# Kernel tuning notes

Hardware: AMD Instinct MI355X
Metric: run time of the kernel (lower is better)

The kernel has to match this reference:

```python
import jax, jax.numpy as jnp
import numpy as np

B, T, D = 8, 4096, 64

def setup_inputs() -> dict:
    key = jax.random.key(0)
    k1, k2 = jax.random.split(key)
    inputs = jax.random.normal(k1, (B, T, D), dtype=jnp.float32)
    # keras 'random_normal' initializer: stddev 0.05
    W = jax.random.normal(k2, (D, D), dtype=jnp.float32) * 0.05
    return {"inputs": inputs, "W": W}

def reference(inputs, W):
    # q = inputs @ W               : [B,T,D]
    # a = q @ inputs^T             : [B,T,T] (no scaling, bias b unused in original)
    # out = softmax(a, -1) @ inputs: [B,T,D]
    q = jnp.einsum('btd,de->bte', inputs, W)
    scores = jnp.einsum('btd,bsd->bts', q, inputs)
    attn = jax.nn.softmax(scores, axis=-1)
    return jnp.einsum('bts,bsd->btd', attn, inputs)
```

## Files before the change

kernel.cpp:

```cpp
#include <hip/hip_runtime.h>

typedef _Float16 f16;
typedef _Float16 f16x8 __attribute__((ext_vector_type(8)));
typedef __bf16 bf16x8 __attribute__((ext_vector_type(8)));
typedef float floatx4 __attribute__((ext_vector_type(4)));
typedef unsigned short u16;

#define B_N   8
#define T_SEQ 4096
#define DIM   64
#define QT    64
#define NIT   32
#define XSTR  72
#define LOG2E 1.44269504f
#define FRAG  512

#if __has_builtin(__builtin_amdgcn_exp2f)
#define EXP2(x) __builtin_amdgcn_exp2f(x)
#else
#define EXP2(x) exp2f(x)
#endif

typedef __attribute__((address_space(1))) const void gvoid;
typedef __attribute__((address_space(3))) void svoid;

__launch_bounds__(256, 4)
__global__ void prep_kernel(const float* __restrict__ X, const float* __restrict__ W,
                            u16* __restrict__ Kswz, u16* __restrict__ Qswz,
                            u16* __restrict__ Vswz) {
  __shared__ __attribute__((aligned(16))) u16 Xs[32 * XSTR];
  __shared__ __attribute__((aligned(16))) u16 Wt[DIM * XSTR];
  __shared__ __attribute__((aligned(16))) u16 Qs[2][16 * XSTR];
  const int tid = threadIdx.x;
  const int lane = tid & 63, w = tid >> 6, qd = lane >> 4, ln = lane & 15;
  const int b = blockIdx.y;
  const int tau = blockIdx.x;
  const long xbase = ((long)b * T_SEQ + tau * 32) * DIM;

  {
    const int r = tid >> 3, c0 = (tid & 7) * 8;
    float v[8];
    *(float4*)&v[0] = *(const float4*)(X + xbase + (long)r * DIM + c0);
    *(float4*)&v[4] = *(const float4*)(X + xbase + (long)r * DIM + c0 + 4);
    u16 h[8];
#pragma unroll
    for (int j = 0; j < 8; j++) h[j] = __builtin_bit_cast(u16, (f16)v[j]);
    *(uint4*)&Xs[r * XSTR + c0] = *(uint4*)&h[0];
    const int r2 = tid >> 2, c2 = (tid & 3) * 16;
    float wv[16];
#pragma unroll
    for (int i = 0; i < 4; i++)
      *(float4*)&wv[i * 4] = *(const float4*)(W + r2 * DIM + c2 + i * 4);
#pragma unroll
    for (int j = 0; j < 16; j++) Wt[(c2 + j) * XSTR + r2] = __builtin_bit_cast(u16, (f16)wv[j]);
  }
  __syncthreads();

  if (w == 0) {
#pragma unroll
    for (int ct = 0; ct < 2; ct++) {
      const int krow = (ln >> 2) * 8 + ct * 4 + (ln & 3);
      const long F = ((long)b * 128 + tau) * 2 + ct;
#pragma unroll
      for (int ks = 0; ks < 2; ks++) {
        f16x8 kv = *(const f16x8*)&Xs[krow * XSTR + ks * 32 + qd * 8];
        *(f16x8*)(Kswz + (F * 2 + ks) * FRAG + lane * 8) = kv;
      }
    }
    {
      const long Cb = (long)b * 4 + 0;
      bf16x8 vv;
#pragma unroll
      for (int j = 0; j < 8; j++) {
        f16 hv = __builtin_bit_cast(f16, Xs[(qd * 8 + j) * XSTR + 0 * 16 + ln]);
        vv[j] = (__bf16)(float)hv;
      }
      *(bf16x8*)(Vswz + (Cb * (T_SEQ / 32) + tau) * FRAG + lane * 8) = vv;
    }
  } else if (w == 1) {
#pragma unroll
    for (int db = 1; db < 4; db++) {
      const long Cb = (long)b * 4 + db;
      bf16x8 vv;
#pragma unroll
      for (int j = 0; j < 8; j++) {
        f16 hv = __builtin_bit_cast(f16, Xs[(qd * 8 + j) * XSTR + db * 16 + ln]);
        vv[j] = (__bf16)(float)hv;
      }
      *(bf16x8*)(Vswz + (Cb * (T_SEQ / 32) + tau) * FRAG + lane * 8) = vv;
    }
  } else {
    const int h2 = w - 2;
    const int rq = h2 * 16;
    floatx4 acc[4];
#pragma unroll
    for (int ct = 0; ct < 4; ct++) acc[ct] = (floatx4)0.0f;
#pragma unroll
    for (int ks = 0; ks < 2; ks++) {
      f16x8 aX = *(const f16x8*)&Xs[(rq + ln) * XSTR + ks * 32 + qd * 8];
#pragma unroll
      for (int ct = 0; ct < 4; ct++) {
        f16x8 bW = *(const f16x8*)&Wt[(ct * 16 + ln) * XSTR + ks * 32 + qd * 8];
        acc[ct] = __builtin_amdgcn_mfma_f32_16x16x32_f16(aX, bW, acc[ct], 0, 0, 0);
      }
    }
#pragma unroll
    for (int ct = 0; ct < 4; ct++)
#pragma unroll
      for (int r = 0; r < 4; r++)
        Qs[h2][(qd * 4 + r) * XSTR + ct * 16 + ln] =
            __builtin_bit_cast(u16, (f16)(acc[ct][r] * LOG2E));
    const long R = (long)b * (T_SEQ / 16) + tau * 2 + h2;
#pragma unroll
    for (int ks = 0; ks < 2; ks++) {
      f16x8 qv = *(const f16x8*)&Qs[h2][ln * XSTR + ks * 32 + qd * 8];
      *(f16x8*)(Qswz + (R * 2 + ks) * FRAG + lane * 8) = qv;
    }
  }
}

__launch_bounds__(512, 4)
__global__ void attn_kernel(const u16* __restrict__ Kswz, const u16* __restrict__ Qswz,
                            const u16* __restrict__ Vswz, float* __restrict__ out) {
  __shared__ __attribute__((aligned(16))) char smem[35840];
  __shared__ float lpart[8][32];
  float* Opart = (float*)smem;

  const int tid = threadIdx.x;
  const int lane = tid & 63;
  const int w = tid >> 6;
  const int qd = lane >> 4;
  const int ln = lane & 15;
  const int wg = w >> 2;
  const int wk = w & 3;
  const int bid = blockIdx.x;
  const int b = bid & 7;
  const int q0 = (bid >> 3) * QT;
  const long bbase = (long)b * T_SEQ * DIM;

  f16x8 aQ[2][2];
#pragma unroll
  for (int rb = 0; rb < 2; rb++)
#pragma unroll
    for (int ks = 0; ks < 2; ks++)
      aQ[rb][ks] = *(const f16x8*)(Qswz +
          (((long)b * (T_SEQ / 16) + (q0 >> 4) + wg * 2 + rb) * 2 + ks) * FRAG + lane * 8);

  const char* gKw = (const char*)Kswz + (long)b * 524288 + (long)w * 2048 + lane * 16;
  const char* gV = (const char*)Vswz + (long)b * 524288 + (long)wk * 1024 + lane * 16;

#define STAGE(bufv, t)                                                                  \
  do {                                                                                  \
    const char* g = gKw + (long)(t) * 16384;                                            \
    char* l = smem + (bufv) * 16384 + w * 2048;                                         \
    __builtin_amdgcn_global_load_lds((gvoid*)(g), (svoid*)(l), 16, 0, 0);               \
    __builtin_amdgcn_global_load_lds((gvoid*)(g + 1024), (svoid*)(l + 1024), 16, 0, 0); \
  } while (0)

  floatx4 O[2][4];
  float lacc[2] = {0.f, 0.f};
#pragma unroll
  for (int rb = 0; rb < 2; rb++)
#pragma unroll
    for (int db = 0; db < 4; db++) O[rb][db] = (floatx4)0.0f;

  STAGE(0, 0);
  __syncthreads();

  int buf = 0;
#pragma unroll 1
  for (int t = 0; t < NIT; t++) {
    bf16x8 bV[4];
#pragma unroll
    for (int db = 0; db < 4; db++)
      bV[db] = *(const bf16x8*)(gV + (long)t * 4096 + (long)db * 131072);

    if (t + 1 < NIT) STAGE(buf ^ 1, t + 1);

    const char* Kb = smem + buf * 16384 + wk * 4096;
    f16x8 bK[2][2];
#pragma unroll
    for (int ct = 0; ct < 2; ct++)
#pragma unroll
      for (int ks = 0; ks < 2; ks++)
        bK[ct][ks] = *(const f16x8*)(Kb + (ct * 2 + ks) * 1024 + lane * 16);

    floatx4 St[2][2];
#pragma unroll
    for (int ct = 0; ct < 2; ct++)
#pragma unroll
      for (int rb = 0; rb < 2; rb++) St[ct][rb] = (floatx4)0.0f;
    __builtin_amdgcn_s_setprio(1);
#pragma unroll
    for (int ks = 0; ks < 2; ks++)
#pragma unroll
      for (int ct = 0; ct < 2; ct++)
#pragma unroll
        for (int rb = 0; rb < 2; rb++)
          St[ct][rb] = __builtin_amdgcn_mfma_f32_16x16x32_f16(bK[ct][ks], aQ[rb][ks], St[ct][rb], 0, 0, 0);
    __builtin_amdgcn_s_setprio(0);

    bf16x8 pk[2];
#pragma unroll
    for (int rb = 0; rb < 2; rb++) {
      float ps = 0.f;
#pragma unroll
      for (int ct = 0; ct < 2; ct++)
#pragma unroll
        for (int r = 0; r < 4; r++) {
          float p = EXP2(St[ct][rb][r]);
          ps += p;
          pk[rb][ct * 4 + r] = (__bf16)p;
        }
      lacc[rb] += ps;
    }

    __builtin_amdgcn_s_setprio(1);
#pragma unroll
    for (int rb = 0; rb < 2; rb++)
#pragma unroll
      for (int db = 0; db < 4; db++)
        O[rb][db] = __builtin_amdgcn_mfma_f32_16x16x32_bf16(pk[rb], bV[db], O[rb][db], 0, 0, 0);
    __builtin_amdgcn_s_setprio(0);

    __syncthreads();
    buf ^= 1;
  }

#pragma unroll
  for (int rb = 0; rb < 2; rb++) {
    float v = lacc[rb];
    v += __shfl_xor(v, 16, 64);
    v += __shfl_xor(v, 32, 64);
    if (qd == 0) lpart[w][rb * 16 + ln] = v;
  }

#pragma unroll
  for (int rb = 0; rb < 2; rb++) {
    __syncthreads();
#pragma unroll
    for (int db = 0; db < 4; db++)
#pragma unroll
      for (int r = 0; r < 4; r++)
        Opart[(w * 16 + qd * 4 + r) * 68 + db * 16 + ln] = O[rb][db][r];
    __syncthreads();
    const int wg2 = tid >> 8;
    const int q2 = (tid >> 4) & 15;
    const int d0 = (tid & 15) * 4;
    float4 s = *(const float4*)&Opart[((wg2 * 4 + 0) * 16 + q2) * 68 + d0];
    const float4 s1 = *(const float4*)&Opart[((wg2 * 4 + 1) * 16 + q2) * 68 + d0];
    const float4 s2 = *(const float4*)&Opart[((wg2 * 4 + 2) * 16 + q2) * 68 + d0];
    const float4 s3 = *(const float4*)&Opart[((wg2 * 4 + 3) * 16 + q2) * 68 + d0];
    float l = lpart[wg2 * 4 + 0][rb * 16 + q2] + lpart[wg2 * 4 + 1][rb * 16 + q2] +
              lpart[wg2 * 4 + 2][rb * 16 + q2] + lpart[wg2 * 4 + 3][rb * 16 + q2];
    const float inv = 1.0f / l;
    float4 o;
    o.x = (s.x + s1.x + s2.x + s3.x) * inv;
    o.y = (s.y + s1.y + s2.y + s3.y) * inv;
    o.z = (s.z + s1.z + s2.z + s3.z) * inv;
    o.w = (s.w + s1.w + s2.w + s3.w) * inv;
    *(float4*)(out + bbase + (long)(q0 + wg2 * 32 + rb * 16 + q2) * DIM + d0) = o;
  }
#undef STAGE
}

extern "C" void kernel_launch(void* const* d_in, const int* in_sizes, int n_in,
                              void* d_out, int out_size, void* d_ws, size_t ws_size,
                              hipStream_t stream) {
  const float* X = (const float*)d_in[0];
  const float* W = (const float*)d_in[1];
  float* out = (float*)d_out;
  const size_t SZ = (size_t)B_N * T_SEQ * DIM * 2;
  u16* Kswz = (u16*)d_ws;
  u16* Qswz = (u16*)((char*)d_ws + SZ);
  u16* Vswz = (u16*)((char*)d_ws + 2 * SZ);
  prep_kernel<<<dim3(T_SEQ / 32, B_N), 256, 0, stream>>>(X, W, Kswz, Qswz, Vswz);
  attn_kernel<<<dim3(B_N * (T_SEQ / QT)), 512, 0, stream>>>(Kswz, Qswz, Vswz, out);
}
```

Measured before the change: 104.6 us.

## Halve attention query tile to 32 rows, one 16-row block per wave

Reduces the per-block query tile from 64 to 32 rows, so each wave handles a single 16-row query block instead of two. The grid doubles to 1024 blocks, which gives more parallelism across CUs and lowers register pressure. In exchange each K/V tile staged into LDS and loaded from global memory is reused by half as many queries, so total K/V traffic doubles, and per-iteration MFMA work per sync shrinks, raising the relative cost of barriers.

```diff
diff --git a/kernel.cpp b/kernel.cpp
--- a/kernel.cpp
+++ b/kernel.cpp
@@ -9,7 +9,7 @@
 #define B_N   8
 #define T_SEQ 4096
 #define DIM   64
-#define QT    64
+#define QT    32
 #define NIT   32
 #define XSTR  72
 #define LOG2E 1.44269504f
@@ -123,7 +123,7 @@
 __global__ void attn_kernel(const u16* __restrict__ Kswz, const u16* __restrict__ Qswz,
                             const u16* __restrict__ Vswz, float* __restrict__ out) {
   __shared__ __attribute__((aligned(16))) char smem[35840];
-  __shared__ float lpart[8][32];
+  __shared__ float lpart[8][16];
   float* Opart = (float*)smem;
 
   const int tid = threadIdx.x;
@@ -131,20 +131,18 @@
   const int w = tid >> 6;
   const int qd = lane >> 4;
   const int ln = lane & 15;
-  const int wg = w >> 2;
+  const int qh = w >> 2;
   const int wk = w & 3;
   const int bid = blockIdx.x;
   const int b = bid & 7;
   const int q0 = (bid >> 3) * QT;
   const long bbase = (long)b * T_SEQ * DIM;
 
-  f16x8 aQ[2][2];
-#pragma unroll
-  for (int rb = 0; rb < 2; rb++)
-#pragma unroll
-    for (int ks = 0; ks < 2; ks++)
-      aQ[rb][ks] = *(const f16x8*)(Qswz +
-          (((long)b * (T_SEQ / 16) + (q0 >> 4) + wg * 2 + rb) * 2 + ks) * FRAG + lane * 8);
+  f16x8 aQ[2];
+#pragma unroll
+  for (int ks = 0; ks < 2; ks++)
+    aQ[ks] = *(const f16x8*)(Qswz +
+        (((long)b * (T_SEQ / 16) + (q0 >> 4) + qh) * 2 + ks) * FRAG + lane * 8);
 
   const char* gKw = (const char*)Kswz + (long)b * 524288 + (long)w * 2048 + lane * 16;
   const char* gV = (const char*)Vswz + (long)b * 524288 + (long)wk * 1024 + lane * 16;
@@ -157,12 +155,10 @@
     __builtin_amdgcn_global_load_lds((gvoid*)(g + 1024), (svoid*)(l + 1024), 16, 0, 0); \
   } while (0)
 
-  floatx4 O[2][4];
-  float lacc[2] = {0.f, 0.f};
-#pragma unroll
-  for (int rb = 0; rb < 2; rb++)
-#pragma unroll
-    for (int db = 0; db < 4; db++) O[rb][db] = (floatx4)0.0f;
+  floatx4 O[4];
+  float lacc = 0.f;
+#pragma unroll
+  for (int db = 0; db < 4; db++) O[db] = (floatx4)0.0f;
 
   STAGE(0, 0);
   __syncthreads();
@@ -185,81 +181,73 @@
       for (int ks = 0; ks < 2; ks++)
         bK[ct][ks] = *(const f16x8*)(Kb + (ct * 2 + ks) * 1024 + lane * 16);
 
-    floatx4 St[2][2];
-#pragma unroll
-    for (int ct = 0; ct < 2; ct++)
-#pragma unroll
-      for (int rb = 0; rb < 2; rb++) St[ct][rb] = (floatx4)0.0f;
+    floatx4 St[2];
+    St[0] = (floatx4)0.0f;
+    St[1] = (floatx4)0.0f;
     __builtin_amdgcn_s_setprio(1);
 #pragma unroll
     for (int ks = 0; ks < 2; ks++)
 #pragma unroll
       for (int ct = 0; ct < 2; ct++)
-#pragma unroll
-        for (int rb = 0; rb < 2; rb++)
-          St[ct][rb] = __builtin_amdgcn_mfma_f32_16x16x32_f16(bK[ct][ks], aQ[rb][ks], St[ct][rb], 0, 0, 0);
+        St[ct] = __builtin_amdgcn_mfma_f32_16x16x32_f16(bK[ct][ks], aQ[ks], St[ct], 0, 0, 0);
     __builtin_amdgcn_s_setprio(0);
 
-    bf16x8 pk[2];
-#pragma unroll
-    for (int rb = 0; rb < 2; rb++) {
+    bf16x8 pk;
+    {
       float ps = 0.f;
 #pragma unroll
       for (int ct = 0; ct < 2; ct++)
 #pragma unroll
         for (int r = 0; r < 4; r++) {
-          float p = EXP2(St[ct][rb][r]);
+          float p = EXP2(St[ct][r]);
           ps += p;
-          pk[rb][ct * 4 + r] = (__bf16)p;
+          pk[ct * 4 + r] = (__bf16)p;
         }
-      lacc[rb] += ps;
+      lacc += ps;
     }
 
     __builtin_amdgcn_s_setprio(1);
 #pragma unroll
-    for (int rb = 0; rb < 2; rb++)
-#pragma unroll
-      for (int db = 0; db < 4; db++)
-        O[rb][db] = __builtin_amdgcn_mfma_f32_16x16x32_bf16(pk[rb], bV[db], O[rb][db], 0, 0, 0);
+    for (int db = 0; db < 4; db++)
+      O[db] = __builtin_amdgcn_mfma_f32_16x16x32_bf16(pk, bV[db], O[db], 0, 0, 0);
     __builtin_amdgcn_s_setprio(0);
 
     __syncthreads();
     buf ^= 1;
   }
 
-#pragma unroll
-  for (int rb = 0; rb < 2; rb++) {
-    float v = lacc[rb];
+  {
+    float v = lacc;
     v += __shfl_xor(v, 16, 64);
     v += __shfl_xor(v, 32, 64);
-    if (qd == 0) lpart[w][rb * 16 + ln] = v;
-  }
-
-#pragma unroll
-  for (int rb = 0; rb < 2; rb++) {
-    __syncthreads();
-#pragma unroll
-    for (int db = 0; db < 4; db++)
-#pragma unroll
-      for (int r = 0; r < 4; r++)
-        Opart[(w * 16 + qd * 4 + r) * 68 + db * 16 + ln] = O[rb][db][r];
-    __syncthreads();
-    const int wg2 = tid >> 8;
-    const int q2 = (tid >> 4) & 15;
+    if (qd == 0) lpart[w][ln] = v;
+  }
+
+  __syncthreads();
+#pragma unroll
+  for (int db = 0; db < 4; db++)
+#pragma unroll
+    for (int r = 0; r < 4; r++)
+      Opart[(w * 16 + qd * 4 + r) * 68 + db * 16 + ln] = O[db][r];
+  __syncthreads();
+  {
+    const int ql = tid >> 4;
     const int d0 = (tid & 15) * 4;
-    float4 s = *(const float4*)&Opart[((wg2 * 4 + 0) * 16 + q2) * 68 + d0];
-    const float4 s1 = *(const float4*)&Opart[((wg2 * 4 + 1) * 16 + q2) * 68 + d0];
-    const float4 s2 = *(const float4*)&Opart[((wg2 * 4 + 2) * 16 + q2) * 68 + d0];
-    const float4 s3 = *(const float4*)&Opart[((wg2 * 4 + 3) * 16 + q2) * 68 + d0];
-    float l = lpart[wg2 * 4 + 0][rb * 16 + q2] + lpart[wg2 * 4 + 1][rb * 16 + q2] +
-              lpart[wg2 * 4 + 2][rb * 16 + q2] + lpart[wg2 * 4 + 3][rb * 16 + q2];
+    const int qh2 = ql >> 4;
+    const int q2 = ql & 15;
+    float4 s = *(const float4*)&Opart[((qh2 * 4 + 0) * 16 + q2) * 68 + d0];
+    const float4 s1 = *(const float4*)&Opart[((qh2 * 4 + 1) * 16 + q2) * 68 + d0];
+    const float4 s2 = *(const float4*)&Opart[((qh2 * 4 + 2) * 16 + q2) * 68 + d0];
+    const float4 s3 = *(const float4*)&Opart[((qh2 * 4 + 3) * 16 + q2) * 68 + d0];
+    float l = lpart[qh2 * 4 + 0][q2] + lpart[qh2 * 4 + 1][q2] +
+              lpart[qh2 * 4 + 2][q2] + lpart[qh2 * 4 + 3][q2];
     const float inv = 1.0f / l;
     float4 o;
     o.x = (s.x + s1.x + s2.x + s3.x) * inv;
     o.y = (s.y + s1.y + s2.y + s3.y) * inv;
     o.z = (s.z + s1.z + s2.z + s3.z) * inv;
     o.w = (s.w + s1.w + s2.w + s3.w) * inv;
-    *(float4*)(out + bbase + (long)(q0 + wg2 * 32 + rb * 16 + q2) * DIM + d0) = o;
+    *(float4*)(out + bbase + (long)(q0 + ql) * DIM + d0) = o;
   }
 #undef STAGE
 }
```

New measurement: 119.6 us. 1.14x slower.

## Split attention key range in two blocks and combine with a reduce kernel

Applied to the files above, without the earlier changes.

Splits each query tile's key/value sweep into two halves processed by separate blocks, doubling the grid from 512 to 1024 blocks. Each block writes unnormalized partial outputs and row sums to workspace, and a new reduce kernel adds the two halves and normalizes. This aims to improve occupancy across the many compute units, since 512 blocks may underfill the GPU. In exchange it adds an extra kernel launch and extra global traffic for the partials. The split relies on the scores being safe to exponentiate without a running max.

```diff
diff --git a/kernel.cpp b/kernel.cpp
--- a/kernel.cpp
+++ b/kernel.cpp
@@ -10,7 +10,6 @@
 #define T_SEQ 4096
 #define DIM   64
 #define QT    64
-#define NIT   32
 #define XSTR  72
 #define LOG2E 1.44269504f
 #define FRAG  512
@@ -119,9 +118,11 @@
   }
 }
 
+template <int SPLIT>
 __launch_bounds__(512, 4)
 __global__ void attn_kernel(const u16* __restrict__ Kswz, const u16* __restrict__ Qswz,
-                            const u16* __restrict__ Vswz, float* __restrict__ out) {
+                            const u16* __restrict__ Vswz, float* __restrict__ out,
+                            float* __restrict__ Op, float* __restrict__ Lp) {
   __shared__ __attribute__((aligned(16))) char smem[35840];
   __shared__ float lpart[8][32];
   float* Opart = (float*)smem;
@@ -135,7 +136,10 @@
   const int wk = w & 3;
   const int bid = blockIdx.x;
   const int b = bid & 7;
-  const int q0 = (bid >> 3) * QT;
+  const int h = SPLIT ? ((bid >> 3) & 1) : 0;
+  const int g = SPLIT ? (bid >> 4) : (bid >> 3);
+  const int q0 = g * QT;
+  const int NITL = SPLIT ? 16 : 32;
   const long bbase = (long)b * T_SEQ * DIM;
 
   f16x8 aQ[2][2];
@@ -146,15 +150,17 @@
       aQ[rb][ks] = *(const f16x8*)(Qswz +
           (((long)b * (T_SEQ / 16) + (q0 >> 4) + wg * 2 + rb) * 2 + ks) * FRAG + lane * 8);
 
-  const char* gKw = (const char*)Kswz + (long)b * 524288 + (long)w * 2048 + lane * 16;
-  const char* gV = (const char*)Vswz + (long)b * 524288 + (long)wk * 1024 + lane * 16;
+  const char* gKw = (const char*)Kswz + (long)b * 524288 + (long)h * 262144 +
+                    (long)w * 2048 + lane * 16;
+  const char* gV = (const char*)Vswz + (long)b * 524288 + (long)h * 65536 +
+                   (long)wk * 1024 + lane * 16;
 
 #define STAGE(bufv, t)                                                                  \
   do {                                                                                  \
-    const char* g = gKw + (long)(t) * 16384;                                            \
-    char* l = smem + (bufv) * 16384 + w * 2048;                                         \
-    __builtin_amdgcn_global_load_lds((gvoid*)(g), (svoid*)(l), 16, 0, 0);               \
-    __builtin_amdgcn_global_load_lds((gvoid*)(g + 1024), (svoid*)(l + 1024), 16, 0, 0); \
+    const char* g_ = gKw + (long)(t) * 16384;                                           \
+    char* l_ = smem + (bufv) * 16384 + w * 2048;                                        \
+    __builtin_amdgcn_global_load_lds((gvoid*)(g_), (svoid*)(l_), 16, 0, 0);             \
+    __builtin_amdgcn_global_load_lds((gvoid*)(g_ + 1024), (svoid*)(l_ + 1024), 16, 0, 0); \
   } while (0)
 
   floatx4 O[2][4];
@@ -169,13 +175,13 @@
 
   int buf = 0;
 #pragma unroll 1
-  for (int t = 0; t < NIT; t++) {
+  for (int t = 0; t < NITL; t++) {
     bf16x8 bV[4];
 #pragma unroll
     for (int db = 0; db < 4; db++)
       bV[db] = *(const bf16x8*)(gV + (long)t * 4096 + (long)db * 131072);
 
-    if (t + 1 < NIT) STAGE(buf ^ 1, t + 1);
+    if (t + 1 < NITL) STAGE(buf ^ 1, t + 1);
 
     const char* Kb = smem + buf * 16384 + wk * 4096;
     f16x8 bK[2][2];
@@ -247,21 +253,55 @@
     const int wg2 = tid >> 8;
     const int q2 = (tid >> 4) & 15;
     const int d0 = (tid & 15) * 4;
+    const int ql = wg2 * 32 + rb * 16 + q2;
     float4 s = *(const float4*)&Opart[((wg2 * 4 + 0) * 16 + q2) * 68 + d0];
     const float4 s1 = *(const float4*)&Opart[((wg2 * 4 + 1) * 16 + q2) * 68 + d0];
     const float4 s2 = *(const float4*)&Opart[((wg2 * 4 + 2) * 16 + q2) * 68 + d0];
     const float4 s3 = *(const float4*)&Opart[((wg2 * 4 + 3) * 16 + q2) * 68 + d0];
     float l = lpart[wg2 * 4 + 0][rb * 16 + q2] + lpart[wg2 * 4 + 1][rb * 16 + q2] +
               lpart[wg2 * 4 + 2][rb * 16 + q2] + lpart[wg2 * 4 + 3][rb * 16 + q2];
-    const float inv = 1.0f / l;
     float4 o;
-    o.x = (s.x + s1.x + s2.x + s3.x) * inv;
-    o.y = (s.y + s1.y + s2.y + s3.y) * inv;
-    o.z = (s.z + s1.z + s2.z + s3.z) * inv;
-    o.w = (s.w + s1.w + s2.w + s3.w) * inv;
-    *(float4*)(out + bbase + (long)(q0 + wg2 * 32 + rb * 16 + q2) * DIM + d0) = o;
+    o.x = s.x + s1.x + s2.x + s3.x;
+    o.y = s.y + s1.y + s2.y + s3.y;
+    o.z = s.z + s1.z + s2.z + s3.z;
+    o.w = s.w + s1.w + s2.w + s3.w;
+    if (SPLIT) {
+      *(float4*)(Op + (long)bid * (QT * DIM) + ql * DIM + d0) = o;
+      if (d0 == 0) Lp[(long)bid * QT + ql] = l;
+    } else {
+      const float inv = 1.0f / l;
+      o.x *= inv; o.y *= inv; o.z *= inv; o.w *= inv;
+      *(float4*)(out + bbase + (long)(q0 + ql) * DIM + d0) = o;
+    }
   }
 #undef STAGE
+}
+
+__launch_bounds__(256, 8)
+__global__ void reduce_kernel(const float* __restrict__ Op, const float* __restrict__ Lp,
+                              float* __restrict__ out) {
+  const int rb = blockIdx.x;
+  const int b = rb & 7, g = rb >> 3;
+  const int bid0 = g * 16 + b;
+  const int bid1 = g * 16 + 8 + b;
+  const long p0 = (long)bid0 * (QT * DIM);
+  const long p1 = (long)bid1 * (QT * DIM);
+  const long obase = ((long)b * T_SEQ + (long)g * QT) * DIM;
+#pragma unroll
+  for (int i = 0; i < 4; i++) {
+    const int lin4 = i * 256 + threadIdx.x;
+    const int q = lin4 >> 4;
+    const int d0 = (lin4 & 15) * 4;
+    float4 a = *(const float4*)(Op + p0 + (long)lin4 * 4);
+    float4 c = *(const float4*)(Op + p1 + (long)lin4 * 4);
+    const float inv = 1.0f / (Lp[(long)bid0 * QT + q] + Lp[(long)bid1 * QT + q]);
+    float4 o;
+    o.x = (a.x + c.x) * inv;
+    o.y = (a.y + c.y) * inv;
+    o.z = (a.z + c.z) * inv;
+    o.w = (a.w + c.w) * inv;
+    *(float4*)(out + obase + (long)q * DIM + d0) = o;
+  }
 }
 
 extern "C" void kernel_launch(void* const* d_in, const int* in_sizes, int n_in,
@@ -271,9 +311,21 @@
   const float* W = (const float*)d_in[1];
   float* out = (float*)d_out;
   const size_t SZ = (size_t)B_N * T_SEQ * DIM * 2;
+  const size_t OPSZ = (size_t)1024 * QT * DIM * 4;
+  const size_t LPSZ = (size_t)1024 * QT * 4;
   u16* Kswz = (u16*)d_ws;
   u16* Qswz = (u16*)((char*)d_ws + SZ);
   u16* Vswz = (u16*)((char*)d_ws + 2 * SZ);
+  float* Op = (float*)((char*)d_ws + 3 * SZ);
+  float* Lp = (float*)((char*)d_ws + 3 * SZ + OPSZ);
+
   prep_kernel<<<dim3(T_SEQ / 32, B_N), 256, 0, stream>>>(X, W, Kswz, Qswz, Vswz);
-  attn_kernel<<<dim3(B_N * (T_SEQ / QT)), 512, 0, stream>>>(Kswz, Qswz, Vswz, out);
+  if (ws_size >= 3 * SZ + OPSZ + LPSZ) {
+    attn_kernel<1><<<dim3(B_N * (T_SEQ / QT) * 2), 512, 0, stream>>>(
+        Kswz, Qswz, Vswz, out, Op, Lp);
+    reduce_kernel<<<dim3(B_N * (T_SEQ / QT)), 256, 0, stream>>>(Op, Lp, out);
+  } else {
+    attn_kernel<0><<<dim3(B_N * (T_SEQ / QT)), 512, 0, stream>>>(
+        Kswz, Qswz, Vswz, out, Op, Lp);
+  }
 }
```

After: 113.0 us. 8.0% more time.
